# Performance work log

Hardware: AMD Instinct MI355X
Metric: run time of the kernel (lower is better)

The kernel has to match this reference:

```python
import jax, jax.numpy as jnp
import numpy as np


def setup_inputs() -> dict:
    key = jax.random.key(0)
    ks = jax.random.split(key, 8)
    bs, slen, d = 16, 2048, 1024
    scale = 1.0 / np.sqrt(d)
    return {
        "query": jax.random.normal(ks[0], (bs, d), jnp.float32),
        "states": jax.random.normal(ks[1], (bs, slen, d), jnp.float32),
        "Wq": jax.random.normal(ks[2], (d, d), jnp.float32) * scale,
        "bq": jax.random.normal(ks[3], (d,), jnp.float32) * 0.01,
        "Wk": jax.random.normal(ks[4], (d, d), jnp.float32) * scale,
        "bk": jax.random.normal(ks[5], (d,), jnp.float32) * 0.01,
        "We": jax.random.normal(ks[6], (2 * d,), jnp.float32) * scale,
        "be": jax.random.normal(ks[7], (1,), jnp.float32) * 0.01,
    }


def reference(query, states, Wq, bq, Wk, bk, We, be):
    d = Wq.shape[1]
    # q: (bs, d); k: (bs, slen, d)
    q = jax.nn.relu(query @ Wq + bq)
    k = jax.nn.relu(jnp.einsum("bsv,vd->bsd", states, Wk) + bk)
    # tanh(cat(q, k)) @ We == tanh(q) @ We[:d] + tanh(k) @ We[d:]
    # (avoids materializing the repeated/concatenated (bs, slen, 2d) tensor)
    We_q, We_k = We[:d], We[d:]
    energy = (jnp.tanh(q) @ We_q)[:, None] + jnp.einsum("bsd,d->bs", jnp.tanh(k), We_k) + be[0]
    attn_weights = jax.nn.softmax(energy, axis=1)  # (bs, slen)
    attn = jnp.einsum("bs,bsd->bd", attn_weights, states)  # weighted sum of values
    return attn_weights, attn
```

## Files before the change

### kernel.cpp

```cpp
#include <hip/hip_runtime.h>
#include <hip/hip_bf16.h>

#define D 1024
#define SLEN 2048
#define BS 16
#define MROWS (BS*SLEN)

typedef __attribute__((ext_vector_type(8))) short short8;
typedef __attribute__((ext_vector_type(4))) float f32x4;

__device__ __forceinline__ short f2bf(float f) {
  __hip_bfloat16 h = __float2bfloat16(f);
  return __builtin_bit_cast(short, h);
}

__global__ __launch_bounds__(256) void wk_prep(const float* __restrict__ Wk,
                                               short* __restrict__ WkT) {
  const int g = blockIdx.x;
  const int t = threadIdx.x;
#pragma unroll
  for (int it = 0; it < 4; ++it) {
    const int n = it*256 + t;
    short8 p;
#pragma unroll
    for (int j = 0; j < 8; ++j)
      p[j] = f2bf(Wk[(size_t)(g*8 + j)*D + n]);
    *(short8*)(WkT + ((size_t)g*D + n)*8) = p;
  }
}

__global__ __launch_bounds__(512, 2) void energy_gemm(
    const float* __restrict__ states, const short* __restrict__ WkT,
    const float* __restrict__ bk, const float* __restrict__ We,
    float* __restrict__ eraw)
{
  __shared__ short Al[64 * 129 * 8];

  const int tid  = threadIdx.x;
  const int w    = tid >> 6;
  const int lane = tid & 63;
  const int quad = lane >> 4;
  const int l16  = lane & 15;
  const int m0   = blockIdx.x * 64;

  {
    const int row = tid >> 3;
    const int u0  = tid & 7;
    const float* Ag = states + (size_t)(m0 + row)*D;
#pragma unroll
    for (int i = 0; i < 16; ++i) {
      const int u = u0 + i*8;
      float4 x0 = *(const float4*)(Ag + u*8);
      float4 x1 = *(const float4*)(Ag + u*8 + 4);
      short8 p;
      p[0]=f2bf(x0.x); p[1]=f2bf(x0.y); p[2]=f2bf(x0.z); p[3]=f2bf(x0.w);
      p[4]=f2bf(x1.x); p[5]=f2bf(x1.y); p[6]=f2bf(x1.z); p[7]=f2bf(x1.w);
      *(short8*)(Al + ((size_t)row*129 + u)*8) = p;
    }
  }
  __syncthreads();

  f32x4 acc[2][4][4];
#pragma unroll
  for (int nc = 0; nc < 2; ++nc)
#pragma unroll
    for (int mi = 0; mi < 4; ++mi)
#pragma unroll
      for (int ni = 0; ni < 4; ++ni)
        acc[nc][mi][ni] = (f32x4){0.f, 0.f, 0.f, 0.f};

  const short* bbase = WkT + ((size_t)quad*D + w*128 + l16)*8;
  const short* abase = Al + ((size_t)l16*129 + quad)*8;

#define LOADB(ks, buf)                                                   \
  {                                                                      \
    const short* bp = bbase + (size_t)(ks)*32768;                        \
    _Pragma("unroll")                                                    \
    for (int nc = 0; nc < 2; ++nc)                                       \
      _Pragma("unroll")                                                  \
      for (int ni = 0; ni < 4; ++ni)                                     \
        buf[nc*4 + ni] = *(const short8*)(bp + nc*512 + ni*128);         \
  }

#define LOADA(ks, buf)                                                   \
  {                                                                      \
    _Pragma("unroll")                                                    \
    for (int mi = 0; mi < 4; ++mi)                                       \
      buf[mi] = *(const short8*)(abase + mi*16512 + (ks)*32);            \
  }

#define MFMAS(fa, fb)                                                    \
  {                                                                      \
    _Pragma("unroll")                                                    \
    for (int nc = 0; nc < 2; ++nc)                                       \
      _Pragma("unroll")                                                  \
      for (int mi = 0; mi < 4; ++mi)                                     \
        _Pragma("unroll")                                                \
        for (int ni = 0; ni < 4; ++ni)                                   \
          acc[nc][mi][ni] = __builtin_amdgcn_mfma_f32_16x16x32_bf16(     \
              fa[mi], fb[nc*4 + ni], acc[nc][mi][ni], 0, 0, 0);          \
  }

  short8 fa0[4], fa1[4], fb0[8], fb1[8];
  LOADA(0, fa0); LOADB(0, fb0);
#pragma unroll
  for (int kk = 0; kk < 16; ++kk) {
    LOADA(2*kk + 1, fa1); LOADB(2*kk + 1, fb1);
    MFMAS(fa0, fb0);
    if (kk < 15) { LOADA(2*kk + 2, fa0); LOADB(2*kk + 2, fb0); }
    MFMAS(fa1, fb1);
  }

  float esum[16];
#pragma unroll
  for (int q = 0; q < 16; ++q) esum[q] = 0.f;
#pragma unroll
  for (int nc = 0; nc < 2; ++nc)
#pragma unroll
    for (int ni = 0; ni < 4; ++ni) {
      const int n = w*128 + nc*64 + ni*16 + l16;
      const float bkv = bk[n];
      const float wev = We[D + n];
#pragma unroll
      for (int mi = 0; mi < 4; ++mi)
#pragma unroll
        for (int r = 0; r < 4; ++r) {
          float x = acc[nc][mi][ni][r] + bkv;
          x = fmaxf(x, 0.f);
          float ex = __expf(2.f * x);
          float th = 1.f - 2.f/(ex + 1.f);
          esum[mi*4 + r] += th * wev;
        }
    }
#pragma unroll
  for (int dd = 1; dd < 16; dd <<= 1)
#pragma unroll
    for (int q = 0; q < 16; ++q)
      esum[q] += __shfl_xor(esum[q], dd, 64);

  __syncthreads();
  float* red = (float*)Al;
  if (l16 == 0) {
#pragma unroll
    for (int mi = 0; mi < 4; ++mi)
#pragma unroll
      for (int r = 0; r < 4; ++r)
        red[(mi*16 + quad*4 + r)*8 + w] = esum[mi*4 + r];
  }
  __syncthreads();
  if (tid < 64) {
    float s = 0.f;
#pragma unroll
    for (int wi = 0; wi < 8; ++wi) s += red[tid*8 + wi];
    eraw[m0 + tid] = s;
  }
#undef LOADB
#undef LOADA
#undef MFMAS
}

__global__ __launch_bounds__(256) void attn_sm_partial(
    const float* __restrict__ states, const float* __restrict__ eraw,
    float* __restrict__ wts, float* __restrict__ part)
{
  const int sc = blockIdx.x;
  const int b  = blockIdx.y;
  const int t  = threadIdx.x;
  __shared__ float red[256];
  __shared__ float wsh[128];

  float v[8];
  float m = -1e30f;
#pragma unroll
  for (int j = 0; j < 8; ++j) {
    v[j] = eraw[(size_t)b*SLEN + j*256 + t];
    m = fmaxf(m, v[j]);
  }
  red[t] = m; __syncthreads();
  for (int s = 128; s > 0; s >>= 1) {
    if (t < s) red[t] = fmaxf(red[t], red[t+s]);
    __syncthreads();
  }
  m = red[0];
  __syncthreads();
  float sum = 0.f;
#pragma unroll
  for (int j = 0; j < 8; ++j) sum += __expf(v[j] - m);
  red[t] = sum; __syncthreads();
  for (int s = 128; s > 0; s >>= 1) {
    if (t < s) red[t] += red[t+s];
    __syncthreads();
  }
  const float inv = 1.f / red[0];

  if (t < 128) {
    const float wv = __expf(eraw[(size_t)b*SLEN + sc*128 + t] - m) * inv;
    wts[(size_t)b*SLEN + sc*128 + t] = wv;
    wsh[t] = wv;
  }
  __syncthreads();

  const float* sp = states + ((size_t)b*SLEN + sc*128)*D + t*4;
  float ax = 0.f, ay = 0.f, az = 0.f, aw = 0.f;
#pragma unroll 8
  for (int s = 0; s < 128; ++s) {
    float4 x = *(const float4*)(sp + (size_t)s*D);
    const float wv = wsh[s];
    ax = fmaf(wv, x.x, ax);
    ay = fmaf(wv, x.y, ay);
    az = fmaf(wv, x.z, az);
    aw = fmaf(wv, x.w, aw);
  }
  float4 o; o.x = ax; o.y = ay; o.z = az; o.w = aw;
  *(float4*)(part + ((size_t)(b*16 + sc))*D + t*4) = o;
}

__global__ __launch_bounds__(256) void attn_final(
    const float* __restrict__ part, float* __restrict__ attn)
{
  const int b = blockIdx.x, t = threadIdx.x;
  float4 s = {0.f, 0.f, 0.f, 0.f};
#pragma unroll
  for (int sc = 0; sc < 16; ++sc) {
    float4 v = *(const float4*)(part + ((size_t)(b*16 + sc))*D + t*4);
    s.x += v.x; s.y += v.y; s.z += v.z; s.w += v.w;
  }
  *(float4*)(attn + (size_t)b*D + t*4) = s;
}

extern "C" void kernel_launch(void* const* d_in, const int* in_sizes, int n_in,
                              void* d_out, int out_size, void* d_ws, size_t ws_size,
                              hipStream_t stream) {
  const float* states = (const float*)d_in[1];
  const float* Wk     = (const float*)d_in[4];
  const float* bk     = (const float*)d_in[5];
  const float* We     = (const float*)d_in[6];
  float* out = (float*)d_out;

  short* WkT  = (short*)d_ws;
  float* part = (float*)((char*)d_ws + (size_t)D*D*sizeof(short));
  float* eraw = (float*)((char*)d_ws + (size_t)D*D*sizeof(short)
                                     + (size_t)BS*16*D*sizeof(float));

  (void)in_sizes; (void)n_in; (void)out_size; (void)ws_size;

  wk_prep<<<128, 256, 0, stream>>>(Wk, WkT);
  energy_gemm<<<MROWS/64, 512, 0, stream>>>(states, WkT, bk, We, eraw);
  attn_sm_partial<<<dim3(16, BS), 256, 0, stream>>>(states, eraw, out, part);
  attn_final<<<BS, 256, 0, stream>>>(part, out + MROWS);
}
```

Baseline: 299.5 us.

## Split softmax into its own kernel and widen the weighted-sum grid

Moves the per-batch softmax into a separate small kernel so the weighted-sum kernel no longer recomputes the full-row max/sum reduction in every block. The weighted-sum pass now uses 64 chunks of 32 rows per batch instead of 16 chunks of 128, which gives 1024 blocks to better saturate memory bandwidth. States reads in the GEMM and the weighted sum use nontemporal loads to reduce cache pollution. In exchange it adds an extra kernel launch, and the final reduction now sums four times as many partial vectors.

```diff
diff --git a/kernel.cpp b/kernel.cpp
--- a/kernel.cpp
+++ b/kernel.cpp
@@ -12,6 +12,11 @@
 __device__ __forceinline__ short f2bf(float f) {
   __hip_bfloat16 h = __float2bfloat16(f);
   return __builtin_bit_cast(short, h);
+}
+
+__device__ __forceinline__ float4 ntload4(const float* p) {
+  f32x4 v = __builtin_nontemporal_load((const f32x4*)p);
+  float4 r; r.x = v.x; r.y = v.y; r.z = v.z; r.w = v.w; return r;
 }
 
 __global__ __launch_bounds__(256) void wk_prep(const float* __restrict__ Wk,
@@ -50,8 +55,8 @@
 #pragma unroll
     for (int i = 0; i < 16; ++i) {
       const int u = u0 + i*8;
-      float4 x0 = *(const float4*)(Ag + u*8);
-      float4 x1 = *(const float4*)(Ag + u*8 + 4);
+      float4 x0 = ntload4(Ag + u*8);
+      float4 x1 = ntload4(Ag + u*8 + 4);
       short8 p;
       p[0]=f2bf(x0.x); p[1]=f2bf(x0.y); p[2]=f2bf(x0.z); p[3]=f2bf(x0.w);
       p[4]=f2bf(x1.x); p[5]=f2bf(x1.y); p[6]=f2bf(x1.z); p[7]=f2bf(x1.w);
@@ -159,52 +164,53 @@
 #undef MFMAS
 }
 
-__global__ __launch_bounds__(256) void attn_sm_partial(
-    const float* __restrict__ states, const float* __restrict__ eraw,
-    float* __restrict__ wts, float* __restrict__ part)
+__global__ __launch_bounds__(256) void softmax_rows(
+    const float* __restrict__ eraw, float* __restrict__ wts) {
+  const int b = blockIdx.x, t = threadIdx.x;
+  __shared__ float red[256];
+  float v[8];
+  float m = -1e30f;
+#pragma unroll
+  for (int j = 0; j < 8; ++j) {
+    v[j] = eraw[(size_t)b*SLEN + j*256 + t];
+    m = fmaxf(m, v[j]);
+  }
+  red[t] = m; __syncthreads();
+  for (int s = 128; s > 0; s >>= 1) {
+    if (t < s) red[t] = fmaxf(red[t], red[t+s]);
+    __syncthreads();
+  }
+  m = red[0];
+  __syncthreads();
+  float sum = 0.f;
+#pragma unroll
+  for (int j = 0; j < 8; ++j) { v[j] = __expf(v[j] - m); sum += v[j]; }
+  red[t] = sum; __syncthreads();
+  for (int s = 128; s > 0; s >>= 1) {
+    if (t < s) red[t] += red[t+s];
+    __syncthreads();
+  }
+  const float inv = 1.f / red[0];
+#pragma unroll
+  for (int j = 0; j < 8; ++j)
+    wts[(size_t)b*SLEN + j*256 + t] = v[j] * inv;
+}
+
+__global__ __launch_bounds__(256) void attn_partial(
+    const float* __restrict__ states, const float* __restrict__ wts,
+    float* __restrict__ part)
 {
   const int sc = blockIdx.x;
   const int b  = blockIdx.y;
   const int t  = threadIdx.x;
-  __shared__ float red[256];
-  __shared__ float wsh[128];
-
-  float v[8];
-  float m = -1e30f;
-#pragma unroll
-  for (int j = 0; j < 8; ++j) {
-    v[j] = eraw[(size_t)b*SLEN + j*256 + t];
-    m = fmaxf(m, v[j]);
-  }
-  red[t] = m; __syncthreads();
-  for (int s = 128; s > 0; s >>= 1) {
-    if (t < s) red[t] = fmaxf(red[t], red[t+s]);
-    __syncthreads();
-  }
-  m = red[0];
-  __syncthreads();
-  float sum = 0.f;
-#pragma unroll
-  for (int j = 0; j < 8; ++j) sum += __expf(v[j] - m);
-  red[t] = sum; __syncthreads();
-  for (int s = 128; s > 0; s >>= 1) {
-    if (t < s) red[t] += red[t+s];
-    __syncthreads();
-  }
-  const float inv = 1.f / red[0];
-
-  if (t < 128) {
-    const float wv = __expf(eraw[(size_t)b*SLEN + sc*128 + t] - m) * inv;
-    wts[(size_t)b*SLEN + sc*128 + t] = wv;
-    wsh[t] = wv;
-  }
-  __syncthreads();
-
-  const float* sp = states + ((size_t)b*SLEN + sc*128)*D + t*4;
+  __shared__ float wsh[32];
+  if (t < 32) wsh[t] = wts[(size_t)b*SLEN + sc*32 + t];
+  __syncthreads();
+  const float* sp = states + ((size_t)b*SLEN + sc*32)*D + t*4;
   float ax = 0.f, ay = 0.f, az = 0.f, aw = 0.f;
-#pragma unroll 8
-  for (int s = 0; s < 128; ++s) {
-    float4 x = *(const float4*)(sp + (size_t)s*D);
+#pragma unroll
+  for (int s = 0; s < 32; ++s) {
+    float4 x = ntload4(sp + (size_t)s*D);
     const float wv = wsh[s];
     ax = fmaf(wv, x.x, ax);
     ay = fmaf(wv, x.y, ay);
@@ -212,7 +218,7 @@
     aw = fmaf(wv, x.w, aw);
   }
   float4 o; o.x = ax; o.y = ay; o.z = az; o.w = aw;
-  *(float4*)(part + ((size_t)(b*16 + sc))*D + t*4) = o;
+  *(float4*)(part + ((size_t)(b*64 + sc))*D + t*4) = o;
 }
 
 __global__ __launch_bounds__(256) void attn_final(
@@ -221,8 +227,8 @@
   const int b = blockIdx.x, t = threadIdx.x;
   float4 s = {0.f, 0.f, 0.f, 0.f};
 #pragma unroll
-  for (int sc = 0; sc < 16; ++sc) {
-    float4 v = *(const float4*)(part + ((size_t)(b*16 + sc))*D + t*4);
+  for (int sc = 0; sc < 64; ++sc) {
+    float4 v = *(const float4*)(part + ((size_t)(b*64 + sc))*D + t*4);
     s.x += v.x; s.y += v.y; s.z += v.z; s.w += v.w;
   }
   *(float4*)(attn + (size_t)b*D + t*4) = s;
@@ -238,14 +244,15 @@
   float* out = (float*)d_out;
 
   short* WkT  = (short*)d_ws;
-  float* part = (float*)((char*)d_ws + (size_t)D*D*sizeof(short));
-  float* eraw = (float*)((char*)d_ws + (size_t)D*D*sizeof(short)
-                                     + (size_t)BS*16*D*sizeof(float));
+  float* eraw = (float*)((char*)d_ws + (size_t)D*D*sizeof(short));
+  float* part = (float*)((char*)d_ws + (size_t)D*D*sizeof(short)
+                                     + (size_t)MROWS*sizeof(float));
 
   (void)in_sizes; (void)n_in; (void)out_size; (void)ws_size;
 
   wk_prep<<<128, 256, 0, stream>>>(Wk, WkT);
   energy_gemm<<<MROWS/64, 512, 0, stream>>>(states, WkT, bk, We, eraw);
-  attn_sm_partial<<<dim3(16, BS), 256, 0, stream>>>(states, eraw, out, part);
+  softmax_rows<<<BS, 256, 0, stream>>>(eraw, out);
+  attn_partial<<<dim3(64, BS), 256, 0, stream>>>(states, out, part);
   attn_final<<<BS, 256, 0, stream>>>(part, out + MROWS);
 }
```

Measured after the change: 294.7 us. Within noise of the previous version (-1.6%).
